# Kernel optimization log

Hardware: AMD Instinct MI355X
Metric: run time of the kernel (lower is better)

The kernel has to match this reference:

```python
import jax, jax.numpy as jnp
import numpy as np

NUM_HEADS = 16


def setup_inputs() -> dict:
    key = jax.random.key(0)
    ks = jax.random.split(key, 8)
    B_, N, C = 2048, 64, 512
    nW = 64
    return {
        "x": jax.random.normal(ks[0], (B_, N, C), dtype=jnp.float32),
        "pe": jax.random.normal(ks[1], (1, N, C), dtype=jnp.float32),
        "rpe": jax.random.normal(ks[2], (NUM_HEADS, N, N), dtype=jnp.float32),
        "mask": jax.random.normal(ks[3], (nW, N, N), dtype=jnp.float32),
        "qkv_w": jax.random.normal(ks[4], (3 * C, C), dtype=jnp.float32) * 0.02,
        "qkv_b": jax.random.normal(ks[5], (3 * C,), dtype=jnp.float32) * 0.02,
        "proj_w": jax.random.normal(ks[6], (C, C), dtype=jnp.float32) * 0.02,
        "proj_b": jax.random.normal(ks[7], (C,), dtype=jnp.float32) * 0.02,
    }


def reference(x, pe, rpe, mask, qkv_w, qkv_b, proj_w, proj_b):
    B_, N, C = x.shape
    H = NUM_HEADS
    hd = C // H
    scale = hd ** -0.5
    xp = x + pe  # (B_, N, C)
    qkv = xp @ qkv_w.T + qkv_b  # (B_, N, 3C)
    qkv = qkv.reshape(B_, N, 3, H, hd).transpose(2, 0, 3, 1, 4)  # (3, B_, H, N, hd)
    q, k, v = qkv[0], qkv[1], qkv[2]
    attn = jnp.einsum("bhnd,bhmd->bhnm", q * scale, k)  # (B_, H, N, N)
    attn = attn + rpe[None]  # broadcast rpe over batch
    nW = mask.shape[0]
    attn = attn.reshape(B_ // nW, nW, H, N, N) + mask[None, :, None]
    attn = attn.reshape(B_, H, N, N)
    attn = jax.nn.softmax(attn, axis=-1)
    out = jnp.einsum("bhnm,bhmd->bhnd", attn, v)  # (B_, H, N, hd)
    out = out.transpose(0, 2, 1, 3).reshape(B_, N, C)
    return out @ proj_w.T + proj_b
```

## Files before the change

### kernel.cpp

```cpp
#include <hip/hip_runtime.h>
#include <hip/hip_bf16.h>
#include <cstdint>

typedef __bf16 bf16;
typedef __bf16 bf16x8_t __attribute__((ext_vector_type(8)));
typedef __bf16 bf16x4_t __attribute__((ext_vector_type(4)));
typedef float  f32x4_t  __attribute__((ext_vector_type(4)));

#define MFMA16(a, b, c) __builtin_amdgcn_mfma_f32_16x16x32_bf16((a), (b), (c), 0, 0, 0)

__device__ __forceinline__ void gload_lds16(const bf16* g, bf16* l) {
    __builtin_amdgcn_global_load_lds(
        (const __attribute__((address_space(1))) void*)g,
        (__attribute__((address_space(3))) void*)l,
        16, 0, 0);
}

__global__ void k_wprep(const float* __restrict__ wq, const float* __restrict__ wp,
                        bf16* __restrict__ wqb, bf16* __restrict__ wpb) {
    int t = blockIdx.x * 256 + threadIdx.x;
    int stride = gridDim.x * 256;
    for (int i = t; i < 196608; i += stride) {
        float4 v = ((const float4*)wq)[i];
        bf16x4_t o; o[0]=(bf16)v.x; o[1]=(bf16)v.y; o[2]=(bf16)v.z; o[3]=(bf16)v.w;
        ((bf16x4_t*)wqb)[i] = o;
    }
    for (int i = t; i < 65536; i += stride) {
        float4 v = ((const float4*)wp)[i];
        bf16x4_t o; o[0]=(bf16)v.x; o[1]=(bf16)v.y; o[2]=(bf16)v.z; o[3]=(bf16)v.w;
        ((bf16x4_t*)wpb)[i] = o;
    }
}

__device__ __forceinline__ void stage_ws(const bf16* __restrict__ wq, bf16* wsbuf,
                                         int h, int kt, int wave, int lane) {
#pragma unroll
    for (int ii = 0; ii < 3; ++ii) {
        int instr = wave * 3 + ii;
        int rr = instr * 4 + (lane >> 4);
        int s  = lane & 15;
        int gp = (s & 8) | ((s & 7) ^ (rr & 7));
        int R  = ((rr >> 5) << 9) + (h << 5) + (rr & 31);
        gload_lds16(wq + (size_t)R * 512 + kt * 128 + gp * 8, wsbuf + instr * 512);
    }
}

__global__ __launch_bounds__(512) void k_qkv_attn(
    const float* __restrict__ x,
    const float* __restrict__ pe,
    const float* __restrict__ rpe,
    const float* __restrict__ mask,
    const float* __restrict__ qkv_b,
    const bf16*  __restrict__ wq,
    bf16* __restrict__ ao)
{
    __shared__ bf16 Ws[2][96 * 128];
    __shared__ bf16 qs[4][64 * 40];
    __shared__ bf16 ks[4][64 * 40];
    __shared__ bf16 vts[4][32 * 72];
    __shared__ bf16 ps[4][64 * 72];

    const int tid  = threadIdx.x;
    const int lane = tid & 63;
    const int wave = tid >> 6;
    const int win  = wave >> 1;
    const int half = wave & 1;
    const int lr   = lane & 15;
    const int lg   = lane >> 4;
    const int row0 = half * 32;
    const int b4   = blockIdx.x * 4 + win;
    const int wi   = b4 & 63;

    bf16x8_t a[2][16];
#pragma unroll
    for (int t = 0; t < 2; ++t) {
        const float* xr = x  + ((size_t)(b4 * 64 + row0 + t * 16 + lr)) * 512;
        const float* pr = pe + (size_t)(row0 + t * 16 + lr) * 512;
#pragma unroll
        for (int kc = 0; kc < 16; ++kc) {
            int k = kc * 32 + lg * 8;
            float4 x0 = *(const float4*)(xr + k);
            float4 x1 = *(const float4*)(xr + k + 4);
            float4 p0 = *(const float4*)(pr + k);
            float4 p1 = *(const float4*)(pr + k + 4);
            bf16x8_t v;
            v[0]=(bf16)(x0.x+p0.x); v[1]=(bf16)(x0.y+p0.y);
            v[2]=(bf16)(x0.z+p0.z); v[3]=(bf16)(x0.w+p0.w);
            v[4]=(bf16)(x1.x+p1.x); v[5]=(bf16)(x1.y+p1.y);
            v[6]=(bf16)(x1.z+p1.z); v[7]=(bf16)(x1.w+p1.w);
            a[t][kc] = v;
        }
    }

    const float SCALE = 0.17677669529663687f;

    stage_ws(wq, Ws[0], 0, 0, wave, lane);

    for (int h = 0; h < 16; ++h) {
        float bpre[6];
#pragma unroll
        for (int j = 0; j < 6; ++j)
            bpre[j] = qkv_b[(j >> 1) * 512 + h * 32 + (j & 1) * 16 + lr];

        f32x4_t acc[2][6] = {};
#pragma unroll
        for (int kt = 0; kt < 4; ++kt) {
            const int ph = h * 4 + kt;
            if (ph < 63) {
                const int pn = ph + 1;
                stage_ws(wq, Ws[(kt + 1) & 1], pn >> 2, pn & 3, wave, lane);
                asm volatile("s_waitcnt vmcnt(3)" ::: "memory");
            } else {
                asm volatile("s_waitcnt vmcnt(0)" ::: "memory");
            }
            __builtin_amdgcn_s_barrier();
#pragma unroll
            for (int k2 = 0; k2 < 4; ++k2) {
                const int kc = kt * 4 + k2;
#pragma unroll
                for (int j = 0; j < 6; ++j) {
                    int row  = j * 16 + lr;
                    int p    = k2 * 4 + lg;
                    int phys = (p & 8) | ((p & 7) ^ (row & 7));
                    bf16x8_t bfrag = *(const bf16x8_t*)&Ws[kt & 1][row * 128 + phys * 8];
                    acc[0][j] = MFMA16(a[0][kc], bfrag, acc[0][j]);
                    acc[1][j] = MFMA16(a[1][kc], bfrag, acc[1][j]);
                }
            }
            asm volatile("s_waitcnt lgkmcnt(0)" ::: "memory");
            __builtin_amdgcn_s_barrier();
        }

#pragma unroll
        for (int t = 0; t < 2; ++t)
#pragma unroll
            for (int j = 0; j < 6; ++j) {
                int which = j >> 1;
                int colh  = (j & 1) * 16 + lr;
#pragma unroll
                for (int r = 0; r < 4; ++r) {
                    int row = row0 + t * 16 + lg * 4 + r;
                    float val = acc[t][j][r] + bpre[j];
                    if (which == 0)      qs[win][row * 40 + colh] = (bf16)val;
                    else if (which == 1) ks[win][row * 40 + colh] = (bf16)val;
                    else                 vts[win][colh * 72 + row] = (bf16)val;
                }
            }
        asm volatile("s_waitcnt lgkmcnt(0)" ::: "memory");
        __builtin_amdgcn_s_barrier();

        const float* rp = rpe  + ((size_t)h)  * 4096;
        const float* mp = mask + ((size_t)wi) * 4096;

#pragma unroll
        for (int t = 0; t < 2; ++t) {
            bf16x8_t aq = *(const bf16x8_t*)&qs[win][(row0 + t * 16 + lr) * 40 + lg * 8];
            f32x4_t s[4];
            f32x4_t zero = {};
#pragma unroll
            for (int j = 0; j < 4; ++j) {
                bf16x8_t bk = *(const bf16x8_t*)&ks[win][(j * 16 + lr) * 40 + lg * 8];
                s[j] = MFMA16(aq, bk, zero);
            }
            float rm[4][4];
#pragma unroll
            for (int j = 0; j < 4; ++j) {
                int col = j * 16 + lr;
#pragma unroll
                for (int r = 0; r < 4; ++r) {
                    int row = row0 + t * 16 + lg * 4 + r;
                    rm[j][r] = rp[row * 64 + col] + mp[row * 64 + col];
                }
            }
            float mx[4] = {-1e30f, -1e30f, -1e30f, -1e30f};
#pragma unroll
            for (int j = 0; j < 4; ++j)
#pragma unroll
                for (int r = 0; r < 4; ++r) {
                    float tv = s[j][r] * SCALE + rm[j][r];
                    s[j][r] = tv;
                    mx[r] = fmaxf(mx[r], tv);
                }
#pragma unroll
            for (int r = 0; r < 4; ++r) {
                float m = mx[r];
                m = fmaxf(m, __shfl_xor(m, 1));
                m = fmaxf(m, __shfl_xor(m, 2));
                m = fmaxf(m, __shfl_xor(m, 4));
                m = fmaxf(m, __shfl_xor(m, 8));
                mx[r] = m;
            }
            float sm[4] = {0.f, 0.f, 0.f, 0.f};
#pragma unroll
            for (int j = 0; j < 4; ++j)
#pragma unroll
                for (int r = 0; r < 4; ++r) {
                    float e = __expf(s[j][r] - mx[r]);
                    s[j][r] = e;
                    sm[r] += e;
                }
#pragma unroll
            for (int r = 0; r < 4; ++r) {
                float ssum = sm[r];
                ssum += __shfl_xor(ssum, 1);
                ssum += __shfl_xor(ssum, 2);
                ssum += __shfl_xor(ssum, 4);
                ssum += __shfl_xor(ssum, 8);
                sm[r] = 1.0f / ssum;
            }
#pragma unroll
            for (int j = 0; j < 4; ++j)
#pragma unroll
                for (int r = 0; r < 4; ++r)
                    ps[win][(row0 + t * 16 + lg * 4 + r) * 72 + j * 16 + lr] = (bf16)s[j][r];

            f32x4_t o[2] = {};
#pragma unroll
            for (int kh = 0; kh < 2; ++kh) {
                bf16x8_t pa = *(const bf16x8_t*)&ps[win][(row0 + t * 16 + lr) * 72 + kh * 32 + lg * 8];
#pragma unroll
                for (int jd = 0; jd < 2; ++jd) {
                    bf16x8_t bv = *(const bf16x8_t*)&vts[win][(jd * 16 + lr) * 72 + kh * 32 + lg * 8];
                    o[jd] = MFMA16(pa, bv, o[jd]);
                }
            }
#pragma unroll
            for (int jd = 0; jd < 2; ++jd)
#pragma unroll
                for (int r = 0; r < 4; ++r) {
                    int row = row0 + t * 16 + lg * 4 + r;
                    ao[((size_t)(b4 * 64 + row)) * 512 + h * 32 + jd * 16 + lr] =
                        (bf16)(o[jd][r] * sm[r]);
                }
        }
    }
}

__global__ __launch_bounds__(256) void k_proj(
    const bf16* __restrict__ A, const bf16* __restrict__ Bw,
    const float* __restrict__ bias, float* __restrict__ C)
{
    __shared__ bf16 As[128 * 72];
    __shared__ bf16 Bs[128 * 72];

    const int tid  = threadIdx.x;
    const int lane = tid & 63;
    const int wave = tid >> 6;
    const int lr = lane & 15, lg = lane >> 4;
    const int wr = wave >> 1, wc = wave & 1;
    const int bid = blockIdx.x;
    const int wg  = (bid & 7) * 512 + (bid >> 3);
    const int mb = wg >> 2, nb = wg & 3;
    const size_t m0 = (size_t)mb * 128;
    const int n0 = nb * 128;

    f32x4_t acc[4][4] = {};

    for (int kt = 0; kt < 8; ++kt) {
        const int k0 = kt * 64;
        bf16x8_t va[4], vb[4];
#pragma unroll
        for (int j = 0; j < 4; ++j) {
            int c = tid + 256 * j;
            int row = c >> 3, i8 = (c & 7) * 8;
            va[j] = *(const bf16x8_t*)(A  + (m0 + row) * 512 + k0 + i8);
            vb[j] = *(const bf16x8_t*)(Bw + (size_t)(n0 + row) * 512 + k0 + i8);
        }
        __syncthreads();
#pragma unroll
        for (int j = 0; j < 4; ++j) {
            int c = tid + 256 * j;
            int row = c >> 3, i8 = (c & 7) * 8;
            *(bf16x8_t*)&As[row * 72 + i8] = va[j];
            *(bf16x8_t*)&Bs[row * 72 + i8] = vb[j];
        }
        __syncthreads();

#pragma unroll
        for (int k2 = 0; k2 < 2; ++k2) {
            bf16x8_t af[4], bfr[4];
#pragma unroll
            for (int i = 0; i < 4; ++i)
                af[i] = *(const bf16x8_t*)&As[(wr * 64 + i * 16 + lr) * 72 + k2 * 32 + lg * 8];
#pragma unroll
            for (int j = 0; j < 4; ++j)
                bfr[j] = *(const bf16x8_t*)&Bs[(wc * 64 + j * 16 + lr) * 72 + k2 * 32 + lg * 8];
#pragma unroll
            for (int i = 0; i < 4; ++i)
#pragma unroll
                for (int j = 0; j < 4; ++j)
                    acc[i][j] = MFMA16(af[i], bfr[j], acc[i][j]);
        }
    }

    float bj[4];
#pragma unroll
    for (int j = 0; j < 4; ++j) bj[j] = bias[n0 + wc * 64 + j * 16 + lr];
#pragma unroll
    for (int i = 0; i < 4; ++i) {
#pragma unroll
        for (int j = 0; j < 4; ++j) {
            int col = n0 + wc * 64 + j * 16 + lr;
#pragma unroll
            for (int r = 0; r < 4; ++r) {
                size_t row = m0 + wr * 64 + i * 16 + lg * 4 + r;
                C[row * 512 + col] = acc[i][j][r] + bj[j];
            }
        }
    }
}

extern "C" void kernel_launch(void* const* d_in, const int* in_sizes, int n_in,
                              void* d_out, int out_size, void* d_ws, size_t ws_size,
                              hipStream_t stream) {
    (void)in_sizes; (void)n_in; (void)out_size; (void)ws_size;
    const float* x      = (const float*)d_in[0];
    const float* pe     = (const float*)d_in[1];
    const float* rpe    = (const float*)d_in[2];
    const float* mask   = (const float*)d_in[3];
    const float* qkv_w  = (const float*)d_in[4];
    const float* qkv_b  = (const float*)d_in[5];
    const float* proj_w = (const float*)d_in[6];
    const float* proj_b = (const float*)d_in[7];
    float* out = (float*)d_out;

    char* ws = (char*)d_ws;
    bf16* wqkvb  = (bf16*)ws;
    bf16* wprojb = (bf16*)(ws + 1572864);
    bf16* ao     = (bf16*)(ws + 2097152);

    k_wprep<<<256, 256, 0, stream>>>(qkv_w, proj_w, wqkvb, wprojb);
    k_qkv_attn<<<512, 512, 0, stream>>>(x, pe, rpe, mask, qkv_b, wqkvb, ao);
    k_proj<<<4096, 256, 0, stream>>>(ao, wprojb, proj_b, out);
}
```

Before: 779.8 us.

## Split fused QKV+attention into a tiled QKV GEMM and a separate attention kernel

New measurement: 994.4 us. 27.5% more time.

```diff
diff --git a/kernel.cpp b/kernel.cpp
--- a/kernel.cpp
+++ b/kernel.cpp
@@ -8,13 +8,6 @@
 typedef float  f32x4_t  __attribute__((ext_vector_type(4)));
 
 #define MFMA16(a, b, c) __builtin_amdgcn_mfma_f32_16x16x32_bf16((a), (b), (c), 0, 0, 0)
-
-__device__ __forceinline__ void gload_lds16(const bf16* g, bf16* l) {
-    __builtin_amdgcn_global_load_lds(
-        (const __attribute__((address_space(1))) void*)g,
-        (__attribute__((address_space(3))) void*)l,
-        16, 0, 0);
-}
 
 __global__ void k_wprep(const float* __restrict__ wq, const float* __restrict__ wp,
                         bf16* __restrict__ wqb, bf16* __restrict__ wpb) {
@@ -32,153 +25,163 @@
     }
 }
 
-__device__ __forceinline__ void stage_ws(const bf16* __restrict__ wq, bf16* wsbuf,
-                                         int h, int kt, int wave, int lane) {
-#pragma unroll
-    for (int ii = 0; ii < 3; ++ii) {
-        int instr = wave * 3 + ii;
-        int rr = instr * 4 + (lane >> 4);
-        int s  = lane & 15;
-        int gp = (s & 8) | ((s & 7) ^ (rr & 7));
-        int R  = ((rr >> 5) << 9) + (h << 5) + (rr & 31);
-        gload_lds16(wq + (size_t)R * 512 + kt * 128 + gp * 8, wsbuf + instr * 512);
-    }
-}
-
-__global__ __launch_bounds__(512) void k_qkv_attn(
+__global__ __launch_bounds__(256, 2) void k_qkv(
     const float* __restrict__ x,
     const float* __restrict__ pe,
-    const float* __restrict__ rpe,
-    const float* __restrict__ mask,
-    const float* __restrict__ qkv_b,
-    const bf16*  __restrict__ wq,
-    bf16* __restrict__ ao)
+    const bf16*  __restrict__ Bw,
+    const float* __restrict__ bias,
+    bf16* __restrict__ Cq)
 {
-    __shared__ bf16 Ws[2][96 * 128];
-    __shared__ bf16 qs[4][64 * 40];
-    __shared__ bf16 ks[4][64 * 40];
-    __shared__ bf16 vts[4][32 * 72];
-    __shared__ bf16 ps[4][64 * 72];
+    __shared__ bf16 As[128 * 72];
+    __shared__ bf16 Bs[128 * 72];
 
     const int tid  = threadIdx.x;
     const int lane = tid & 63;
     const int wave = tid >> 6;
-    const int win  = wave >> 1;
-    const int half = wave & 1;
-    const int lr   = lane & 15;
-    const int lg   = lane >> 4;
-    const int row0 = half * 32;
-    const int b4   = blockIdx.x * 4 + win;
-    const int wi   = b4 & 63;
-
-    bf16x8_t a[2][16];
-#pragma unroll
-    for (int t = 0; t < 2; ++t) {
-        const float* xr = x  + ((size_t)(b4 * 64 + row0 + t * 16 + lr)) * 512;
-        const float* pr = pe + (size_t)(row0 + t * 16 + lr) * 512;
-#pragma unroll
-        for (int kc = 0; kc < 16; ++kc) {
-            int k = kc * 32 + lg * 8;
-            float4 x0 = *(const float4*)(xr + k);
-            float4 x1 = *(const float4*)(xr + k + 4);
-            float4 p0 = *(const float4*)(pr + k);
-            float4 p1 = *(const float4*)(pr + k + 4);
+    const int lr = lane & 15, lg = lane >> 4;
+    const int wr = wave >> 1, wc = wave & 1;
+    const int bid = blockIdx.x;
+    const int wg  = (bid & 7) * 768 + (bid >> 3);
+    const int mb  = wg / 12, nb = wg - mb * 12;
+    const size_t m0 = (size_t)mb * 128;
+    const int n0 = nb * 128;
+
+    f32x4_t acc[4][4] = {};
+
+    for (int kt = 0; kt < 8; ++kt) {
+        const int k0 = kt * 64;
+        bf16x8_t va[4], vb[4];
+#pragma unroll
+        for (int j = 0; j < 4; ++j) {
+            int c = tid + 256 * j;
+            int row = c >> 3, i8 = (c & 7) * 8;
+            const float* xr = x  + (m0 + row) * 512 + k0 + i8;
+            const float* pr = pe + (size_t)(row & 63) * 512 + k0 + i8;
+            float4 x0 = *(const float4*)(xr);
+            float4 x1 = *(const float4*)(xr + 4);
+            float4 p0 = *(const float4*)(pr);
+            float4 p1 = *(const float4*)(pr + 4);
             bf16x8_t v;
             v[0]=(bf16)(x0.x+p0.x); v[1]=(bf16)(x0.y+p0.y);
             v[2]=(bf16)(x0.z+p0.z); v[3]=(bf16)(x0.w+p0.w);
             v[4]=(bf16)(x1.x+p1.x); v[5]=(bf16)(x1.y+p1.y);
             v[6]=(bf16)(x1.z+p1.z); v[7]=(bf16)(x1.w+p1.w);
-            a[t][kc] = v;
-        }
-    }
+            va[j] = v;
+            vb[j] = *(const bf16x8_t*)(Bw + (size_t)(n0 + row) * 512 + k0 + i8);
+        }
+        __syncthreads();
+#pragma unroll
+        for (int j = 0; j < 4; ++j) {
+            int c = tid + 256 * j;
+            int row = c >> 3, i8 = (c & 7) * 8;
+            *(bf16x8_t*)&As[row * 72 + i8] = va[j];
+            *(bf16x8_t*)&Bs[row * 72 + i8] = vb[j];
+        }
+        __syncthreads();
+
+#pragma unroll
+        for (int k2 = 0; k2 < 2; ++k2) {
+            bf16x8_t af[4], bfr[4];
+#pragma unroll
+            for (int i = 0; i < 4; ++i)
+                af[i] = *(const bf16x8_t*)&As[(wr * 64 + i * 16 + lr) * 72 + k2 * 32 + lg * 8];
+#pragma unroll
+            for (int j = 0; j < 4; ++j)
+                bfr[j] = *(const bf16x8_t*)&Bs[(wc * 64 + j * 16 + lr) * 72 + k2 * 32 + lg * 8];
+#pragma unroll
+            for (int i = 0; i < 4; ++i)
+#pragma unroll
+                for (int j = 0; j < 4; ++j)
+                    acc[i][j] = MFMA16(af[i], bfr[j], acc[i][j]);
+        }
+    }
+
+    float bj[4];
+#pragma unroll
+    for (int j = 0; j < 4; ++j) bj[j] = bias[n0 + wc * 64 + j * 16 + lr];
+#pragma unroll
+    for (int i = 0; i < 4; ++i)
+#pragma unroll
+        for (int j = 0; j < 4; ++j) {
+            int col = n0 + wc * 64 + j * 16 + lr;
+#pragma unroll
+            for (int r = 0; r < 4; ++r) {
+                size_t row = m0 + wr * 64 + i * 16 + lg * 4 + r;
+                Cq[row * 1536 + col] = (bf16)(acc[i][j][r] + bj[j]);
+            }
+        }
+}
+
+__global__ __launch_bounds__(256, 2) void k_attn(
+    const bf16*  __restrict__ qkv,
+    const float* __restrict__ rpe,
+    const float* __restrict__ mask,
+    bf16* __restrict__ ao,
+    int winbase)
+{
+    __shared__ bf16 vts[4][32 * 72];
+    __shared__ bf16 ps[4][64 * 72];
+
+    const int tid  = threadIdx.x;
+    const int lane = tid & 63;
+    const int wave = tid >> 6;
+    const int lr   = lane & 15;
+    const int lg   = lane >> 4;
+    const int bw   = blockIdx.x;
+    const int gw   = winbase + bw;
+    const int wi   = gw & 63;
+    const size_t qbase = (size_t)bw * 64 * 1536;
+    const float* mp = mask + (size_t)wi * 4096;
+    bf16* pvt = &vts[wave][0];
+    bf16* pps = &ps[wave][0];
 
     const float SCALE = 0.17677669529663687f;
 
-    stage_ws(wq, Ws[0], 0, 0, wave, lane);
-
-    for (int h = 0; h < 16; ++h) {
-        float bpre[6];
-#pragma unroll
-        for (int j = 0; j < 6; ++j)
-            bpre[j] = qkv_b[(j >> 1) * 512 + h * 32 + (j & 1) * 16 + lr];
-
-        f32x4_t acc[2][6] = {};
-#pragma unroll
-        for (int kt = 0; kt < 4; ++kt) {
-            const int ph = h * 4 + kt;
-            if (ph < 63) {
-                const int pn = ph + 1;
-                stage_ws(wq, Ws[(kt + 1) & 1], pn >> 2, pn & 3, wave, lane);
-                asm volatile("s_waitcnt vmcnt(3)" ::: "memory");
-            } else {
-                asm volatile("s_waitcnt vmcnt(0)" ::: "memory");
-            }
-            __builtin_amdgcn_s_barrier();
-#pragma unroll
-            for (int k2 = 0; k2 < 4; ++k2) {
-                const int kc = kt * 4 + k2;
-#pragma unroll
-                for (int j = 0; j < 6; ++j) {
-                    int row  = j * 16 + lr;
-                    int p    = k2 * 4 + lg;
-                    int phys = (p & 8) | ((p & 7) ^ (row & 7));
-                    bf16x8_t bfrag = *(const bf16x8_t*)&Ws[kt & 1][row * 128 + phys * 8];
-                    acc[0][j] = MFMA16(a[0][kc], bfrag, acc[0][j]);
-                    acc[1][j] = MFMA16(a[1][kc], bfrag, acc[1][j]);
-                }
-            }
-            asm volatile("s_waitcnt lgkmcnt(0)" ::: "memory");
-            __builtin_amdgcn_s_barrier();
-        }
-
-#pragma unroll
-        for (int t = 0; t < 2; ++t)
-#pragma unroll
-            for (int j = 0; j < 6; ++j) {
-                int which = j >> 1;
-                int colh  = (j & 1) * 16 + lr;
-#pragma unroll
-                for (int r = 0; r < 4; ++r) {
-                    int row = row0 + t * 16 + lg * 4 + r;
-                    float val = acc[t][j][r] + bpre[j];
-                    if (which == 0)      qs[win][row * 40 + colh] = (bf16)val;
-                    else if (which == 1) ks[win][row * 40 + colh] = (bf16)val;
-                    else                 vts[win][colh * 72 + row] = (bf16)val;
-                }
-            }
-        asm volatile("s_waitcnt lgkmcnt(0)" ::: "memory");
-        __builtin_amdgcn_s_barrier();
-
-        const float* rp = rpe  + ((size_t)h)  * 4096;
-        const float* mp = mask + ((size_t)wi) * 4096;
-
-#pragma unroll
-        for (int t = 0; t < 2; ++t) {
-            bf16x8_t aq = *(const bf16x8_t*)&qs[win][(row0 + t * 16 + lr) * 40 + lg * 8];
+    for (int hh = 0; hh < 4; ++hh) {
+        const int h  = wave * 4 + hh;
+        const int hc = h * 32;
+        const float* rp = rpe + (size_t)h * 4096;
+
+        bf16x8_t qf[4], kf[4];
+#pragma unroll
+        for (int t = 0; t < 4; ++t) {
+            qf[t] = *(const bf16x8_t*)(qkv + qbase + (size_t)(t * 16 + lr) * 1536 + hc + lg * 8);
+            kf[t] = *(const bf16x8_t*)(qkv + qbase + (size_t)(t * 16 + lr) * 1536 + 512 + hc + lg * 8);
+        }
+#pragma unroll
+        for (int j = 0; j < 4; ++j) {
+            bf16x8_t vr = *(const bf16x8_t*)(qkv + qbase +
+                (size_t)(j * 16 + (lane >> 2)) * 1536 + 1024 + hc + (lane & 3) * 8);
+#pragma unroll
+            for (int i = 0; i < 8; ++i)
+                pvt[((lane & 3) * 8 + i) * 72 + j * 16 + (lane >> 2)] = vr[i];
+        }
+
+        float sminv[4][4];
+#pragma unroll
+        for (int mt = 0; mt < 4; ++mt) {
             f32x4_t s[4];
             f32x4_t zero = {};
 #pragma unroll
-            for (int j = 0; j < 4; ++j) {
-                bf16x8_t bk = *(const bf16x8_t*)&ks[win][(j * 16 + lr) * 40 + lg * 8];
-                s[j] = MFMA16(aq, bk, zero);
-            }
+            for (int nt = 0; nt < 4; ++nt)
+                s[nt] = MFMA16(qf[mt], kf[nt], zero);
             float rm[4][4];
 #pragma unroll
-            for (int j = 0; j < 4; ++j) {
-                int col = j * 16 + lr;
+            for (int nt = 0; nt < 4; ++nt) {
+                int col = nt * 16 + lr;
 #pragma unroll
                 for (int r = 0; r < 4; ++r) {
-                    int row = row0 + t * 16 + lg * 4 + r;
-                    rm[j][r] = rp[row * 64 + col] + mp[row * 64 + col];
+                    int row = mt * 16 + lg * 4 + r;
+                    rm[nt][r] = rp[row * 64 + col] + mp[row * 64 + col];
                 }
             }
             float mx[4] = {-1e30f, -1e30f, -1e30f, -1e30f};
 #pragma unroll
-            for (int j = 0; j < 4; ++j)
+            for (int nt = 0; nt < 4; ++nt)
 #pragma unroll
                 for (int r = 0; r < 4; ++r) {
-                    float tv = s[j][r] * SCALE + rm[j][r];
-                    s[j][r] = tv;
+                    float tv = s[nt][r] * SCALE + rm[nt][r];
+                    s[nt][r] = tv;
                     mx[r] = fmaxf(mx[r], tv);
                 }
 #pragma unroll
@@ -192,11 +195,11 @@
             }
             float sm[4] = {0.f, 0.f, 0.f, 0.f};
 #pragma unroll
-            for (int j = 0; j < 4; ++j)
+            for (int nt = 0; nt < 4; ++nt)
 #pragma unroll
                 for (int r = 0; r < 4; ++r) {
-                    float e = __expf(s[j][r] - mx[r]);
-                    s[j][r] = e;
+                    float e = __expf(s[nt][r] - mx[r]);
+                    s[nt][r] = e;
                     sm[r] += e;
                 }
 #pragma unroll
@@ -206,21 +209,24 @@
                 ssum += __shfl_xor(ssum, 2);
                 ssum += __shfl_xor(ssum, 4);
                 ssum += __shfl_xor(ssum, 8);
-                sm[r] = 1.0f / ssum;
-            }
-#pragma unroll
-            for (int j = 0; j < 4; ++j)
+                sminv[mt][r] = 1.0f / ssum;
+            }
+#pragma unroll
+            for (int nt = 0; nt < 4; ++nt)
 #pragma unroll
                 for (int r = 0; r < 4; ++r)
-                    ps[win][(row0 + t * 16 + lg * 4 + r) * 72 + j * 16 + lr] = (bf16)s[j][r];
-
+                    pps[(mt * 16 + lg * 4 + r) * 72 + nt * 16 + lr] = (bf16)s[nt][r];
+        }
+
+#pragma unroll
+        for (int mt = 0; mt < 4; ++mt) {
             f32x4_t o[2] = {};
 #pragma unroll
-            for (int kh = 0; kh < 2; ++kh) {
-                bf16x8_t pa = *(const bf16x8_t*)&ps[win][(row0 + t * 16 + lr) * 72 + kh * 32 + lg * 8];
+            for (int ks = 0; ks < 2; ++ks) {
+                bf16x8_t pa = *(const bf16x8_t*)&pps[(mt * 16 + lr) * 72 + ks * 32 + lg * 8];
 #pragma unroll
                 for (int jd = 0; jd < 2; ++jd) {
-                    bf16x8_t bv = *(const bf16x8_t*)&vts[win][(jd * 16 + lr) * 72 + kh * 32 + lg * 8];
+                    bf16x8_t bv = *(const bf16x8_t*)&pvt[(jd * 16 + lr) * 72 + ks * 32 + lg * 8];
                     o[jd] = MFMA16(pa, bv, o[jd]);
                 }
             }
@@ -228,9 +234,8 @@
             for (int jd = 0; jd < 2; ++jd)
 #pragma unroll
                 for (int r = 0; r < 4; ++r) {
-                    int row = row0 + t * 16 + lg * 4 + r;
-                    ao[((size_t)(b4 * 64 + row)) * 512 + h * 32 + jd * 16 + lr] =
-                        (bf16)(o[jd][r] * sm[r]);
+                    size_t row = (size_t)gw * 64 + mt * 16 + lg * 4 + r;
+                    ao[row * 512 + hc + jd * 16 + lr] = (bf16)(o[jd][r] * sminv[mt][r]);
                 }
         }
     }
@@ -297,7 +302,7 @@
 #pragma unroll
     for (int j = 0; j < 4; ++j) bj[j] = bias[n0 + wc * 64 + j * 16 + lr];
 #pragma unroll
-    for (int i = 0; i < 4; ++i) {
+    for (int i = 0; i < 4; ++i)
 #pragma unroll
         for (int j = 0; j < 4; ++j) {
             int col = n0 + wc * 64 + j * 16 + lr;
@@ -307,7 +312,6 @@
                 C[row * 512 + col] = acc[i][j][r] + bj[j];
             }
         }
-    }
 }
 
 extern "C" void kernel_launch(void* const* d_in, const int* in_sizes, int n_in,
@@ -318,8 +322,8 @@
     const float* pe     = (const float*)d_in[1];
     const float* rpe    = (const float*)d_in[2];
     const float* mask   = (const float*)d_in[3];
+    const float* qkv_b  = (const float*)d_in[5];
     const float* qkv_w  = (const float*)d_in[4];
-    const float* qkv_b  = (const float*)d_in[5];
     const float* proj_w = (const float*)d_in[6];
     const float* proj_b = (const float*)d_in[7];
     float* out = (float*)d_out;
@@ -328,8 +332,13 @@
     bf16* wqkvb  = (bf16*)ws;
     bf16* wprojb = (bf16*)(ws + 1572864);
     bf16* ao     = (bf16*)(ws + 2097152);
+    bf16* qkvscr = (bf16*)d_out;
 
     k_wprep<<<256, 256, 0, stream>>>(qkv_w, proj_w, wqkvb, wprojb);
-    k_qkv_attn<<<512, 512, 0, stream>>>(x, pe, rpe, mask, qkv_b, wqkvb, ao);
+    for (int pass = 0; pass < 2; ++pass) {
+        k_qkv<<<6144, 256, 0, stream>>>(x + (size_t)pass * 65536 * 512, pe,
+                                        wqkvb, qkv_b, qkvscr);
+        k_attn<<<1024, 256, 0, stream>>>(qkvscr, rpe, mask, ao, pass * 1024);
+    }
     k_proj<<<4096, 256, 0, stream>>>(ao, wprojb, proj_b, out);
 }
```
